# Kernel optimization log

Hardware: AMD Instinct MI355X
Metric: run time of the kernel (lower is better)

Reference implementation:

```python
import jax, jax.numpy as jnp
import numpy as np

D = 3          # matrix dimension (fixed in source)
WIDTH = 23     # hidden channel width (fixed in source)
B = 524288     # batch of 3x3 symmetric matrices

# layer channel dims: {1:1}->{1:W}, W->W, W->W, W->1
_LAYER_DIMS = [(1, WIDTH), (WIDTH, WIDTH), (WIDTH, WIDTH), (WIDTH, 1)]


def setup_inputs() -> dict:
    key = jax.random.key(0)
    ks = jax.random.split(key, 1 + 3 * len(_LAYER_DIMS))
    a = jax.random.normal(ks[0], (B, D, D), dtype=jnp.float32)
    x = a + jnp.swapaxes(a, -1, -2)  # symmetric inputs, as eigh expects
    inp = {"x": x}
    for li, (ic, oc) in enumerate(_LAYER_DIMS):
        s = 1.0 / np.sqrt(2.0 * ic * D)
        inp[f"w_id{li}"] = (jax.random.normal(ks[1 + 3 * li], (oc, ic)) * s).astype(jnp.float32)
        inp[f"w_sum{li}"] = (jax.random.normal(ks[2 + 3 * li], (oc, ic)) * s).astype(jnp.float32)
        inp[f"b{li}"] = jnp.zeros((oc,), dtype=jnp.float32)
    return inp


def _perm_layer(t, w_id, w_sum, b):
    # t: (B, in_c, D). S_D-equivariant linear map on order-1 tensors:
    # identity basis + all-ones(sum) basis + constant-vector bias.
    y = jnp.einsum('oc,bcd->bod', w_id, t)
    y = y + jnp.einsum('oc,bc->bo', w_sum, t.sum(-1))[:, :, None]
    return y + b[None, :, None]


def reference(x, w_id0, w_sum0, b0, w_id1, w_sum1, b1,
              w_id2, w_sum2, b2, w_id3, w_sum3, b3):
    evals, evecs = jnp.linalg.eigh(x)          # (B,D), (B,D,D)
    t = evals[:, None, :]                      # (B,1,D)
    layers = [(w_id0, w_sum0, b0), (w_id1, w_sum1, b1),
              (w_id2, w_sum2, b2), (w_id3, w_sum3, b3)]
    for i, (wi, ws, b) in enumerate(layers):
        t = _perm_layer(t, wi, ws, b)
        if i < len(layers) - 1:
            t = jax.nn.relu(t)
    ev = t[:, 0, :]                            # (B,D) transformed eigenvalues
    # eigvecs @ diag(ev) @ eigvecs^T, batched
    return jnp.einsum('bik,bk,bjk->bij', evecs, ev, evecs)
```

## Files before the change

kernel.cpp:

```cpp
#include <hip/hip_runtime.h>
#include <math.h>


#define MLP_W 23
#define NCP   12

typedef _Float16 h2   __attribute__((ext_vector_type(2)));
typedef _Float16 f16x4 __attribute__((ext_vector_type(4)));
typedef _Float16 f16x8 __attribute__((ext_vector_type(8)));
typedef float    f32x4 __attribute__((ext_vector_type(4)));

__device__ __attribute__((aligned(16))) h2 g_afrag[2][2][2][64][4];
__device__ h2 g_w3[2 * NCP];

__global__ void svh_prep_kernel(const float* __restrict__ wi1, const float* __restrict__ ws1,
                                const float* __restrict__ wi2, const float* __restrict__ ws2,
                                const float* __restrict__ wi3, const float* __restrict__ ws3) {
    int t = blockIdx.x * blockDim.x + threadIdx.x;
    if (t < 512) {
        int lane  = t & 63;
        int mt    = (t >> 6) & 1;
        int mat   = (t >> 7) & 1;
        int layer = (t >> 8) & 1;
        const float* W = layer ? (mat ? ws2 : wi2) : (mat ? ws1 : wi1);
        int row = mt * 16 + (lane & 15);
        int g   = lane >> 4;
#pragma unroll
        for (int dw = 0; dw < 4; ++dw) {
            int k0 = 8 * g + 2 * dw, k1 = k0 + 1;
            float a = (row < MLP_W && k0 < MLP_W) ? W[row * MLP_W + k0] : 0.0f;
            float b = (row < MLP_W && k1 < MLP_W) ? W[row * MLP_W + k1] : 0.0f;
            g_afrag[layer][mat][mt][lane][dw] = (h2){(_Float16)a, (_Float16)b};
        }
    }
    if (t < NCP) {
        int c0 = 2 * t, c1 = 2 * t + 1;
        float wia = wi3[c0], wsa = ws3[c0];
        float wib = (c1 < MLP_W) ? wi3[c1] : 0.0f;
        float wsb = (c1 < MLP_W) ? ws3[c1] : 0.0f;
        g_w3[2 * t]     = (h2){(_Float16)wia, (_Float16)wib};
        g_w3[2 * t + 1] = (h2){(_Float16)wsa, (_Float16)wsb};
    }
}

__device__ __forceinline__ float sinv(float d) {
    return (fabsf(d) > 1e-20f) ? (1.0f / d) : 0.0f;
}

__device__ __forceinline__ f32x4 mm16(f16x8 a, f16x8 b) {
    return __builtin_amdgcn_mfma_f32_16x16x32_f16(a, b, (f32x4){0.f, 0.f, 0.f, 0.f}, 0, 0, 0);
}

#define COL_STRIDE 56
#define CHB   (64 * COL_STRIDE)
#define ZOFF  (4 * CHB)
#define LDSZ  (ZOFF + 16)

__global__ __launch_bounds__(64, 3)
void svh_eig_mlp_kernel(
    const float* __restrict__ x,
    const float* __restrict__ wi0, const float* __restrict__ ws0, const float* __restrict__ bb0,
    const float* __restrict__ bb1, const float* __restrict__ bb2, const float* __restrict__ bb3,
    float* __restrict__ out, int B)
{
    __shared__ alignas(16) unsigned char lds[LDSZ];

    const int lane = threadIdx.x;
    const int g    = lane >> 4;
    int idx  = blockIdx.x * 64 + lane;
    int cidx = (idx < B) ? idx : (B - 1);

    const float* xp = x + (size_t)cidx * 9;
    float x00 = xp[0], x01 = xp[1], x02 = xp[2];
    float x11 = xp[4], x12 = xp[5], x22 = xp[8];

    if (lane < 2) *(f16x4*)(lds + ZOFF + 8 * lane) = (f16x4){0, 0, 0, 0};

    float q   = (x00 + x11 + x22) * (1.0f / 3.0f);
    float a00 = x00 - q, a11 = x11 - q, a22 = x22 - q;
    float p1  = x01 * x01 + x02 * x02 + x12 * x12;
    float p2  = a00 * a00 + a11 * a11 + a22 * a22 + 2.0f * p1;
    float p   = sqrtf(p2 * (1.0f / 6.0f));
    float ip  = sinv(p);
    float d00 = a00 * ip, d11 = a11 * ip, d22 = a22 * ip;
    float c01 = x01 * ip, c02 = x02 * ip, c12 = x12 * ip;
    float detB = d00 * (d11 * d22 - c12 * c12)
               - c01 * (c01 * d22 - c12 * c02)
               + c02 * (c01 * c12 - d11 * c02);
    float r = 0.5f * detB;
    r = fminf(1.0f, fmaxf(-1.0f, r));
    float phi  = acosf(r) * (1.0f / 3.0f);
    float cph  = __cosf(phi);
    float sph  = sqrtf(fmaxf(0.0f, 1.0f - cph * cph));
    const float SQ3 = 1.7320508075688772f;
    float lc = q + 2.0f * p * cph;
    float la = q - p * cph - SQ3 * p * sph;
    float lb = q - p * cph + SQ3 * p * sph;

    f16x8 Afr[2][2][2];
#pragma unroll
    for (int L = 0; L < 2; ++L)
#pragma unroll
        for (int m = 0; m < 2; ++m)
#pragma unroll
            for (int mt = 0; mt < 2; ++mt)
                Afr[L][m][mt] = *(const f16x8*)(&g_afrag[L][m][mt][lane][0]);

    float breg[2][2][4];
#pragma unroll
    for (int L = 0; L < 2; ++L) {
        const float* bb = L ? bb2 : bb1;
#pragma unroll
        for (int mt = 0; mt < 2; ++mt)
#pragma unroll
            for (int rr = 0; rr < 4; ++rr) {
                int row = mt * 16 + 4 * g + rr;
                breg[L][mt][rr] = (row < MLP_W) ? bb[row] : 0.0f;
            }
    }

    {
        float S = la + lb + lc;
        const int base = lane * COL_STRIDE;
#pragma unroll
        for (int m = 0; m < 6; ++m) {
            float t0[4], t1[4], t2[4], ts[4];
#pragma unroll
            for (int rr = 0; rr < 4; ++rr) {
                int o = 4 * m + rr;
                if (o < MLP_W) {
                    float wiv = wi0[o];
                    float u   = fmaf(ws0[o], S, bb0[o]);
                    t0[rr] = fmaxf(0.0f, fmaf(wiv, la, u));
                    t1[rr] = fmaxf(0.0f, fmaf(wiv, lb, u));
                    t2[rr] = fmaxf(0.0f, fmaf(wiv, lc, u));
                } else { t0[rr] = t1[rr] = t2[rr] = 0.0f; }
                ts[rr] = t0[rr] + t1[rr] + t2[rr];
            }
            f16x4 v0 = {(_Float16)t0[0], (_Float16)t0[1], (_Float16)t0[2], (_Float16)t0[3]};
            f16x4 v1 = {(_Float16)t1[0], (_Float16)t1[1], (_Float16)t1[2], (_Float16)t1[3]};
            f16x4 v2 = {(_Float16)t2[0], (_Float16)t2[1], (_Float16)t2[2], (_Float16)t2[3]};
            f16x4 vs = {(_Float16)ts[0], (_Float16)ts[1], (_Float16)ts[2], (_Float16)ts[3]};
            *(f16x4*)(lds + 0 * CHB + base + 8 * m) = v0;
            *(f16x4*)(lds + 1 * CHB + base + 8 * m) = v1;
            *(f16x4*)(lds + 2 * CHB + base + 8 * m) = v2;
            *(f16x4*)(lds + 3 * CHB + base + 8 * m) = vs;
        }
    }

#pragma unroll
    for (int L = 0; L < 2; ++L) {
        __syncthreads();
#pragma unroll
        for (int pp = 0; pp < 4; ++pp) {
            const int colb = (16 * pp + (lane & 15)) * COL_STRIDE;
            f16x8 bf[4];
#pragma unroll
            for (int h = 0; h < 4; ++h) {
                int off = (g == 3) ? ZOFF : (h * CHB + colb + g * 16);
                f16x4 lo = *(const f16x4*)(lds + off);
                f16x4 hi = *(const f16x4*)(lds + off + 8);
                bf[h] = __builtin_shufflevector(lo, hi, 0, 1, 2, 3, 4, 5, 6, 7);
            }
            f32x4 a0m0 = mm16(Afr[L][0][0], bf[0]);
            f32x4 a0m1 = mm16(Afr[L][0][1], bf[0]);
            f32x4 a1m0 = mm16(Afr[L][0][0], bf[1]);
            f32x4 a1m1 = mm16(Afr[L][0][1], bf[1]);
            f32x4 a2m0 = mm16(Afr[L][0][0], bf[2]);
            f32x4 a2m1 = mm16(Afr[L][0][1], bf[2]);
            f32x4 asm0 = mm16(Afr[L][1][0], bf[3]);
            f32x4 asm1 = mm16(Afr[L][1][1], bf[3]);

#pragma unroll
            for (int mt = 0; mt < 2; ++mt) {
                if (mt == 1 && g >= 2) continue;
                f32x4 c0 = (mt == 0) ? a0m0 : a0m1;
                f32x4 c1 = (mt == 0) ? a1m0 : a1m1;
                f32x4 c2 = (mt == 0) ? a2m0 : a2m1;
                f32x4 cs = (mt == 0) ? asm0 : asm1;
                float y0[4], y1[4], y2[4], sn[4];
#pragma unroll
                for (int rr = 0; rr < 4; ++rr) {
                    float u  = cs[rr] + breg[L][mt][rr];
                    float v0 = fmaxf(0.0f, c0[rr] + u);
                    float v1 = fmaxf(0.0f, c1[rr] + u);
                    float v2 = fmaxf(0.0f, c2[rr] + u);
                    y0[rr] = v0; y1[rr] = v1; y2[rr] = v2;
                    sn[rr] = v0 + v1 + v2;
                }
                int wb = colb + mt * 32 + 8 * g;
                f16x4 w0 = {(_Float16)y0[0], (_Float16)y0[1], (_Float16)y0[2], (_Float16)y0[3]};
                f16x4 w1 = {(_Float16)y1[0], (_Float16)y1[1], (_Float16)y1[2], (_Float16)y1[3]};
                f16x4 w2 = {(_Float16)y2[0], (_Float16)y2[1], (_Float16)y2[2], (_Float16)y2[3]};
                f16x4 w3 = {(_Float16)sn[0], (_Float16)sn[1], (_Float16)sn[2], (_Float16)sn[3]};
                *(f16x4*)(lds + 0 * CHB + wb) = w0;
                *(f16x4*)(lds + 1 * CHB + wb) = w1;
                *(f16x4*)(lds + 2 * CHB + wb) = w2;
                *(f16x4*)(lds + 3 * CHB + wb) = w3;
            }
        }
    }
    __syncthreads();

    float eva, evb, evc;
    {
        float a0 = 0.f, a1 = 0.f, a2 = 0.f, as = 0.f;
        const int base = lane * COL_STRIDE;
#pragma unroll
        for (int m = 0; m < 6; ++m) {
            f16x4 q0 = *(const f16x4*)(lds + 0 * CHB + base + 8 * m);
            f16x4 q1 = *(const f16x4*)(lds + 1 * CHB + base + 8 * m);
            f16x4 q2 = *(const f16x4*)(lds + 2 * CHB + base + 8 * m);
            f16x4 qs = *(const f16x4*)(lds + 3 * CHB + base + 8 * m);
            h2 wia = g_w3[4 * m],     wsa = g_w3[4 * m + 1];
            h2 wib = g_w3[4 * m + 2], wsb = g_w3[4 * m + 3];
            a0 = __builtin_amdgcn_fdot2(wia, __builtin_shufflevector(q0, q0, 0, 1), a0, false);
            a0 = __builtin_amdgcn_fdot2(wib, __builtin_shufflevector(q0, q0, 2, 3), a0, false);
            a1 = __builtin_amdgcn_fdot2(wia, __builtin_shufflevector(q1, q1, 0, 1), a1, false);
            a1 = __builtin_amdgcn_fdot2(wib, __builtin_shufflevector(q1, q1, 2, 3), a1, false);
            a2 = __builtin_amdgcn_fdot2(wia, __builtin_shufflevector(q2, q2, 0, 1), a2, false);
            a2 = __builtin_amdgcn_fdot2(wib, __builtin_shufflevector(q2, q2, 2, 3), a2, false);
            as = __builtin_amdgcn_fdot2(wsa, __builtin_shufflevector(qs, qs, 0, 1), as, false);
            as = __builtin_amdgcn_fdot2(wsb, __builtin_shufflevector(qs, qs, 2, 3), as, false);
        }
        float b3v = bb3[0];
        eva = a0 + as + b3v;
        evb = a1 + as + b3v;
        evc = a2 + as + b3v;
    }

    float g1 = (evb - eva) * sinv(lb - la);
    float g2 = (evc - evb) * sinv(lc - lb);
    float c2 = (g2 - g1) * sinv(lc - la);

    float m100 = x00 - la, m111 = x11 - la, m122 = x22 - la;
    float m200 = x00 - lb, m211 = x11 - lb, m222 = x22 - lb;

    float P00 = m100 * m200 + x01 * x01 + x02 * x02;
    float P01 = m100 * x01 + x01 * m211 + x02 * x12;
    float P02 = m100 * x02 + x01 * x12 + x02 * m222;
    float P11 = x01 * x01 + m111 * m211 + x12 * x12;
    float P12 = x01 * x02 + m111 * x12 + x12 * m222;
    float P22 = x02 * x02 + x12 * x12 + m122 * m222;

    float o00 = fmaf(g1, m100, eva) + c2 * P00;
    float o01 = g1 * x01 + c2 * P01;
    float o02 = g1 * x02 + c2 * P02;
    float o11 = fmaf(g1, m111, eva) + c2 * P11;
    float o12 = g1 * x12 + c2 * P12;
    float o22 = fmaf(g1, m122, eva) + c2 * P22;

    if (idx < B) {
        float* op = out + (size_t)idx * 9;
        op[0] = o00; op[1] = o01; op[2] = o02;
        op[3] = o01; op[4] = o11; op[5] = o12;
        op[6] = o02; op[7] = o12; op[8] = o22;
    }
}

extern "C" void kernel_launch(void* const* d_in, const int* in_sizes, int n_in,
                              void* d_out, int out_size, void* d_ws, size_t ws_size,
                              hipStream_t stream) {
    const float* x   = (const float*)d_in[0];
    const float* wi0 = (const float*)d_in[1];
    const float* ws0 = (const float*)d_in[2];
    const float* b0  = (const float*)d_in[3];
    const float* wi1 = (const float*)d_in[4];
    const float* ws1 = (const float*)d_in[5];
    const float* b1  = (const float*)d_in[6];
    const float* wi2 = (const float*)d_in[7];
    const float* ws2 = (const float*)d_in[8];
    const float* b2  = (const float*)d_in[9];
    const float* wi3 = (const float*)d_in[10];
    const float* ws3 = (const float*)d_in[11];
    const float* b3  = (const float*)d_in[12];

    int B = in_sizes[0] / 9;
    float* out = (float*)d_out;

    {
        dim3 block(256);
        dim3 grid(2);
        hipLaunchKernelGGL(svh_prep_kernel, grid, block, 0, stream,
                           wi1, ws1, wi2, ws2, wi3, ws3);
    }

    dim3 block(64);
    dim3 grid((B + 63) / 64);
    hipLaunchKernelGGL(svh_eig_mlp_kernel, grid, block, 0, stream,
                       x, wi0, ws0, b0, b1, b2, b3,
                       out, B);
}
```

Baseline: 122.9 us.

## Fold channel-sum into MFMA accumulation and run final layer on MFMA

Drops the separate summed-channel LDS plane. The sum-basis term is now computed by chaining three accumulating MFMAs over the three eigen-channels. The final 23→1 layer becomes an MFMA over a padded weight fragment, with results redistributed through lane shuffles, replacing the per-lane fdot2 loop and the trailing LDS pass. Weight fragments and biases are loaded per layer instead of all up front, the single-wave workgroup no longer issues barriers, and launch bounds request 4 blocks per CU. This cuts LDS footprint, LDS traffic and register pressure, at the cost of extra MFMA issues for the sum term and for the last layer.

```diff
diff --git a/kernel.cpp b/kernel.cpp
--- a/kernel.cpp
+++ b/kernel.cpp
@@ -3,15 +3,14 @@
 
 
 #define MLP_W 23
-#define NCP   12
-
-typedef _Float16 h2   __attribute__((ext_vector_type(2)));
+
+typedef _Float16 h2    __attribute__((ext_vector_type(2)));
 typedef _Float16 f16x4 __attribute__((ext_vector_type(4)));
 typedef _Float16 f16x8 __attribute__((ext_vector_type(8)));
 typedef float    f32x4 __attribute__((ext_vector_type(4)));
 
 __device__ __attribute__((aligned(16))) h2 g_afrag[2][2][2][64][4];
-__device__ h2 g_w3[2 * NCP];
+__device__ __attribute__((aligned(16))) h2 g_a3frag[64][4];
 
 __global__ void svh_prep_kernel(const float* __restrict__ wi1, const float* __restrict__ ws1,
                                 const float* __restrict__ wi2, const float* __restrict__ ws2,
@@ -33,13 +32,23 @@
             g_afrag[layer][mat][mt][lane][dw] = (h2){(_Float16)a, (_Float16)b};
         }
     }
-    if (t < NCP) {
-        int c0 = 2 * t, c1 = 2 * t + 1;
-        float wia = wi3[c0], wsa = ws3[c0];
-        float wib = (c1 < MLP_W) ? wi3[c1] : 0.0f;
-        float wsb = (c1 < MLP_W) ? ws3[c1] : 0.0f;
-        g_w3[2 * t]     = (h2){(_Float16)wia, (_Float16)wib};
-        g_w3[2 * t + 1] = (h2){(_Float16)wsa, (_Float16)wsb};
+    if (t < 64) {
+        int lane = t;
+        int row  = lane & 15;
+        int g    = lane >> 4;
+#pragma unroll
+        for (int dw = 0; dw < 4; ++dw) {
+            int k0 = 8 * g + 2 * dw, k1 = k0 + 1;
+            float a = 0.0f, b = 0.0f;
+            if (row == 0) {
+                a = (k0 < MLP_W) ? wi3[k0] : 0.0f;
+                b = (k1 < MLP_W) ? wi3[k1] : 0.0f;
+            } else if (row == 1) {
+                a = (k0 < MLP_W) ? ws3[k0] : 0.0f;
+                b = (k1 < MLP_W) ? ws3[k1] : 0.0f;
+            }
+            g_a3frag[lane][dw] = (h2){(_Float16)a, (_Float16)b};
+        }
     }
 }
 
@@ -50,13 +59,16 @@
 __device__ __forceinline__ f32x4 mm16(f16x8 a, f16x8 b) {
     return __builtin_amdgcn_mfma_f32_16x16x32_f16(a, b, (f32x4){0.f, 0.f, 0.f, 0.f}, 0, 0, 0);
 }
+__device__ __forceinline__ f32x4 mm16a(f16x8 a, f16x8 b, f32x4 c) {
+    return __builtin_amdgcn_mfma_f32_16x16x32_f16(a, b, c, 0, 0, 0);
+}
 
 #define COL_STRIDE 56
 #define CHB   (64 * COL_STRIDE)
-#define ZOFF  (4 * CHB)
+#define ZOFF  (3 * CHB)
 #define LDSZ  (ZOFF + 16)
 
-__global__ __launch_bounds__(64, 3)
+__global__ __launch_bounds__(64, 4)
 void svh_eig_mlp_kernel(
     const float* __restrict__ x,
     const float* __restrict__ wi0, const float* __restrict__ ws0, const float* __restrict__ bb0,
@@ -67,6 +79,7 @@
 
     const int lane = threadIdx.x;
     const int g    = lane >> 4;
+    const int c16  = lane & 15;
     int idx  = blockIdx.x * 64 + lane;
     int cidx = (idx < B) ? idx : (B - 1);
 
@@ -97,34 +110,12 @@
     float la = q - p * cph - SQ3 * p * sph;
     float lb = q - p * cph + SQ3 * p * sph;
 
-    f16x8 Afr[2][2][2];
-#pragma unroll
-    for (int L = 0; L < 2; ++L)
-#pragma unroll
-        for (int m = 0; m < 2; ++m)
-#pragma unroll
-            for (int mt = 0; mt < 2; ++mt)
-                Afr[L][m][mt] = *(const f16x8*)(&g_afrag[L][m][mt][lane][0]);
-
-    float breg[2][2][4];
-#pragma unroll
-    for (int L = 0; L < 2; ++L) {
-        const float* bb = L ? bb2 : bb1;
-#pragma unroll
-        for (int mt = 0; mt < 2; ++mt)
-#pragma unroll
-            for (int rr = 0; rr < 4; ++rr) {
-                int row = mt * 16 + 4 * g + rr;
-                breg[L][mt][rr] = (row < MLP_W) ? bb[row] : 0.0f;
-            }
-    }
-
     {
         float S = la + lb + lc;
         const int base = lane * COL_STRIDE;
 #pragma unroll
         for (int m = 0; m < 6; ++m) {
-            float t0[4], t1[4], t2[4], ts[4];
+            float t0[4], t1[4], t2[4];
 #pragma unroll
             for (int rr = 0; rr < 4; ++rr) {
                 int o = 4 * m + rr;
@@ -135,98 +126,110 @@
                     t1[rr] = fmaxf(0.0f, fmaf(wiv, lb, u));
                     t2[rr] = fmaxf(0.0f, fmaf(wiv, lc, u));
                 } else { t0[rr] = t1[rr] = t2[rr] = 0.0f; }
-                ts[rr] = t0[rr] + t1[rr] + t2[rr];
             }
             f16x4 v0 = {(_Float16)t0[0], (_Float16)t0[1], (_Float16)t0[2], (_Float16)t0[3]};
             f16x4 v1 = {(_Float16)t1[0], (_Float16)t1[1], (_Float16)t1[2], (_Float16)t1[3]};
             f16x4 v2 = {(_Float16)t2[0], (_Float16)t2[1], (_Float16)t2[2], (_Float16)t2[3]};
-            f16x4 vs = {(_Float16)ts[0], (_Float16)ts[1], (_Float16)ts[2], (_Float16)ts[3]};
             *(f16x4*)(lds + 0 * CHB + base + 8 * m) = v0;
             *(f16x4*)(lds + 1 * CHB + base + 8 * m) = v1;
             *(f16x4*)(lds + 2 * CHB + base + 8 * m) = v2;
-            *(f16x4*)(lds + 3 * CHB + base + 8 * m) = vs;
-        }
-    }
+        }
+    }
+
+    const f16x8 A3 = *(const f16x8*)(&g_a3frag[lane][0]);
+
+    float eva = 0.0f, evb = 0.0f, evc = 0.0f;
 
 #pragma unroll
     for (int L = 0; L < 2; ++L) {
-        __syncthreads();
+        f16x8 WiM0 = *(const f16x8*)(&g_afrag[L][0][0][lane][0]);
+        f16x8 WiM1 = *(const f16x8*)(&g_afrag[L][0][1][lane][0]);
+        f16x8 WsM0 = *(const f16x8*)(&g_afrag[L][1][0][lane][0]);
+        f16x8 WsM1 = *(const f16x8*)(&g_afrag[L][1][1][lane][0]);
+        const float* bb = L ? bb2 : bb1;
+        float breg[2][4];
+#pragma unroll
+        for (int mt = 0; mt < 2; ++mt)
+#pragma unroll
+            for (int rr = 0; rr < 4; ++rr) {
+                int row = mt * 16 + 4 * g + rr;
+                breg[mt][rr] = (row < MLP_W) ? bb[row] : 0.0f;
+            }
+
 #pragma unroll
         for (int pp = 0; pp < 4; ++pp) {
-            const int colb = (16 * pp + (lane & 15)) * COL_STRIDE;
-            f16x8 bf[4];
-#pragma unroll
-            for (int h = 0; h < 4; ++h) {
+            const int colb = (16 * pp + c16) * COL_STRIDE;
+            f16x8 bf[3];
+#pragma unroll
+            for (int h = 0; h < 3; ++h) {
                 int off = (g == 3) ? ZOFF : (h * CHB + colb + g * 16);
                 f16x4 lo = *(const f16x4*)(lds + off);
                 f16x4 hi = *(const f16x4*)(lds + off + 8);
                 bf[h] = __builtin_shufflevector(lo, hi, 0, 1, 2, 3, 4, 5, 6, 7);
             }
-            f32x4 a0m0 = mm16(Afr[L][0][0], bf[0]);
-            f32x4 a0m1 = mm16(Afr[L][0][1], bf[0]);
-            f32x4 a1m0 = mm16(Afr[L][0][0], bf[1]);
-            f32x4 a1m1 = mm16(Afr[L][0][1], bf[1]);
-            f32x4 a2m0 = mm16(Afr[L][0][0], bf[2]);
-            f32x4 a2m1 = mm16(Afr[L][0][1], bf[2]);
-            f32x4 asm0 = mm16(Afr[L][1][0], bf[3]);
-            f32x4 asm1 = mm16(Afr[L][1][1], bf[3]);
+            f32x4 c0m0 = mm16(WiM0, bf[0]);
+            f32x4 c0m1 = mm16(WiM1, bf[0]);
+            f32x4 c1m0 = mm16(WiM0, bf[1]);
+            f32x4 c1m1 = mm16(WiM1, bf[1]);
+            f32x4 c2m0 = mm16(WiM0, bf[2]);
+            f32x4 c2m1 = mm16(WiM1, bf[2]);
+            f32x4 sm0 = mm16a(WsM0, bf[2], mm16a(WsM0, bf[1], mm16(WsM0, bf[0])));
+            f32x4 sm1 = mm16a(WsM1, bf[2], mm16a(WsM1, bf[1], mm16(WsM1, bf[0])));
 
 #pragma unroll
             for (int mt = 0; mt < 2; ++mt) {
                 if (mt == 1 && g >= 2) continue;
-                f32x4 c0 = (mt == 0) ? a0m0 : a0m1;
-                f32x4 c1 = (mt == 0) ? a1m0 : a1m1;
-                f32x4 c2 = (mt == 0) ? a2m0 : a2m1;
-                f32x4 cs = (mt == 0) ? asm0 : asm1;
-                float y0[4], y1[4], y2[4], sn[4];
+                f32x4 c0 = (mt == 0) ? c0m0 : c0m1;
+                f32x4 c1 = (mt == 0) ? c1m0 : c1m1;
+                f32x4 c2 = (mt == 0) ? c2m0 : c2m1;
+                f32x4 cs = (mt == 0) ? sm0  : sm1;
+                float y0[4], y1[4], y2[4];
 #pragma unroll
                 for (int rr = 0; rr < 4; ++rr) {
-                    float u  = cs[rr] + breg[L][mt][rr];
-                    float v0 = fmaxf(0.0f, c0[rr] + u);
-                    float v1 = fmaxf(0.0f, c1[rr] + u);
-                    float v2 = fmaxf(0.0f, c2[rr] + u);
-                    y0[rr] = v0; y1[rr] = v1; y2[rr] = v2;
-                    sn[rr] = v0 + v1 + v2;
+                    float u  = cs[rr] + breg[mt][rr];
+                    y0[rr] = fmaxf(0.0f, c0[rr] + u);
+                    y1[rr] = fmaxf(0.0f, c1[rr] + u);
+                    y2[rr] = fmaxf(0.0f, c2[rr] + u);
                 }
                 int wb = colb + mt * 32 + 8 * g;
                 f16x4 w0 = {(_Float16)y0[0], (_Float16)y0[1], (_Float16)y0[2], (_Float16)y0[3]};
                 f16x4 w1 = {(_Float16)y1[0], (_Float16)y1[1], (_Float16)y1[2], (_Float16)y1[3]};
                 f16x4 w2 = {(_Float16)y2[0], (_Float16)y2[1], (_Float16)y2[2], (_Float16)y2[3]};
-                f16x4 w3 = {(_Float16)sn[0], (_Float16)sn[1], (_Float16)sn[2], (_Float16)sn[3]};
                 *(f16x4*)(lds + 0 * CHB + wb) = w0;
                 *(f16x4*)(lds + 1 * CHB + wb) = w1;
                 *(f16x4*)(lds + 2 * CHB + wb) = w2;
-                *(f16x4*)(lds + 3 * CHB + wb) = w3;
-            }
-        }
-    }
-    __syncthreads();
-
-    float eva, evb, evc;
+            }
+
+            if (L == 1) {
+                f16x8 b2f[3];
+#pragma unroll
+                for (int h = 0; h < 3; ++h) {
+                    int off = (g == 3) ? ZOFF : (h * CHB + colb + g * 16);
+                    f16x4 lo = *(const f16x4*)(lds + off);
+                    f16x4 hi = *(const f16x4*)(lds + off + 8);
+                    b2f[h] = __builtin_shufflevector(lo, hi, 0, 1, 2, 3, 4, 5, 6, 7);
+                }
+                f32x4 D0 = mm16(A3, b2f[0]);
+                f32x4 D1 = mm16(A3, b2f[1]);
+                f32x4 D2 = mm16(A3, b2f[2]);
+                float ssum = D0[1] + D1[1] + D2[1];
+                float ea = D0[0] + ssum;
+                float eb = D1[0] + ssum;
+                float ec = D2[0] + ssum;
+                ea = __shfl(ea, c16);
+                eb = __shfl(eb, c16);
+                ec = __shfl(ec, c16);
+                bool own = (g == pp);
+                eva = own ? ea : eva;
+                evb = own ? eb : evb;
+                evc = own ? ec : evc;
+            }
+        }
+    }
+
     {
-        float a0 = 0.f, a1 = 0.f, a2 = 0.f, as = 0.f;
-        const int base = lane * COL_STRIDE;
-#pragma unroll
-        for (int m = 0; m < 6; ++m) {
-            f16x4 q0 = *(const f16x4*)(lds + 0 * CHB + base + 8 * m);
-            f16x4 q1 = *(const f16x4*)(lds + 1 * CHB + base + 8 * m);
-            f16x4 q2 = *(const f16x4*)(lds + 2 * CHB + base + 8 * m);
-            f16x4 qs = *(const f16x4*)(lds + 3 * CHB + base + 8 * m);
-            h2 wia = g_w3[4 * m],     wsa = g_w3[4 * m + 1];
-            h2 wib = g_w3[4 * m + 2], wsb = g_w3[4 * m + 3];
-            a0 = __builtin_amdgcn_fdot2(wia, __builtin_shufflevector(q0, q0, 0, 1), a0, false);
-            a0 = __builtin_amdgcn_fdot2(wib, __builtin_shufflevector(q0, q0, 2, 3), a0, false);
-            a1 = __builtin_amdgcn_fdot2(wia, __builtin_shufflevector(q1, q1, 0, 1), a1, false);
-            a1 = __builtin_amdgcn_fdot2(wib, __builtin_shufflevector(q1, q1, 2, 3), a1, false);
-            a2 = __builtin_amdgcn_fdot2(wia, __builtin_shufflevector(q2, q2, 0, 1), a2, false);
-            a2 = __builtin_amdgcn_fdot2(wib, __builtin_shufflevector(q2, q2, 2, 3), a2, false);
-            as = __builtin_amdgcn_fdot2(wsa, __builtin_shufflevector(qs, qs, 0, 1), as, false);
-            as = __builtin_amdgcn_fdot2(wsb, __builtin_shufflevector(qs, qs, 2, 3), as, false);
-        }
         float b3v = bb3[0];
-        eva = a0 + as + b3v;
-        evb = a1 + as + b3v;
-        evc = a2 + as + b3v;
+        eva += b3v; evb += b3v; evc += b3v;
     }
 
     float g1 = (evb - eva) * sinv(lb - la);
```

After: 119.6 us. 1.03x faster.
